# Kernel optimization log

Measured on AMD Instinct MI355X. Metric: run time of the kernel, lower is better.

Reference implementation:

```python
import math
import jax, jax.numpy as jnp
import numpy as np

B, T, D = 2, 2048, 1024
H, DH = 16, 64
DFF = int(4 * D * 2 / 3)  # 2730, as in the torch __init__
EPS = 1e-5


def _alibi_slopes(n_heads):
    def p2(n):
        start = 2 ** (-2 ** (-(math.log2(n) - 3)))
        return [start * start ** i for i in range(n)]
    if math.log2(n_heads).is_integer():
        s = p2(n_heads)
    else:
        closest = 2 ** math.floor(math.log2(n_heads))
        s = p2(closest) + p2(2 * closest)[0::2][: n_heads - closest]
    return jnp.asarray(s, dtype=jnp.float32)


def rmsnorm(x, g):
    var = jnp.mean(x * x, axis=-1, keepdims=True)
    return g * (x * jax.lax.rsqrt(var + EPS))


def setup_inputs() -> dict:
    key = jax.random.key(0)
    ks = jax.random.split(key, 9)
    sd = 0.02
    return {
        "x":  jax.random.normal(ks[0], (B, T, D), jnp.float32),
        "g1": jnp.ones((D,), jnp.float32),
        "Wq": jax.random.normal(ks[1], (D, H * DH), jnp.float32) * sd,
        "Wk": jax.random.normal(ks[2], (D, H * DH), jnp.float32) * sd,
        "Wv": jax.random.normal(ks[3], (D, H * DH), jnp.float32) * sd,
        "Wo": jax.random.normal(ks[4], (H * DH, D), jnp.float32) * sd,
        "g2": jnp.ones((D,), jnp.float32),
        "W1": jax.random.normal(ks[5], (D, DFF), jnp.float32) * sd,
        "W2": jax.random.normal(ks[6], (D, DFF), jnp.float32) * sd,
        "W3": jax.random.normal(ks[7], (DFF, D), jnp.float32) * sd,
    }


def reference(x, g1, Wq, Wk, Wv, Wo, g2, W1, W2, W3):
    scale = DH ** -0.5
    h = rmsnorm(x, g1)
    q = (h @ Wq).reshape(B, T, H, DH)
    k = (h @ Wk).reshape(B, T, H, DH)
    v = (h @ Wv).reshape(B, T, H, DH)
    # scores (B, H, T, T)
    att = jnp.einsum("bqhd,bkhd->bhqk", q, k) * scale
    # ALiBi bias as in source: dist = clamp(j - i, min=0) -> zero on causal region
    pos = jnp.arange(T)
    dist = jnp.clip(pos[None, :] - pos[:, None], 0, None).astype(jnp.float32)
    bias = -_alibi_slopes(H)[:, None, None] * dist[None, :, :]  # (H, T, T)
    causal = pos[None, :] <= pos[:, None]  # (T, T)
    neg_inf = jnp.asarray(-jnp.inf, att.dtype)
    att = jnp.where(causal[None, None], att + bias[None], neg_inf)
    p = jax.nn.softmax(att, axis=-1)
    ctx = jnp.einsum("bhqk,bkhd->bqhd", p, v).reshape(B, T, H * DH)
    x = x + ctx @ Wo
    h2 = rmsnorm(x, g2)
    x = x + (jax.nn.silu(h2 @ W1) * (h2 @ W2)) @ W3
    return x
```

## Files before the change

kernel.cpp:

```cpp
#include <hip/hip_runtime.h>
#include <hip/hip_bf16.h>
#include <cstdint>
#include <cstddef>

typedef __bf16 bf16;
typedef __attribute__((ext_vector_type(8))) __bf16 bf16x8;
typedef __attribute__((ext_vector_type(4))) float f32x4;

#define NB 2
#define NT 2048
#define ND 1024
#define NH 16
#define NDH 64
#define NBT 4096
#define NDFF 2730
#define NDFFP 2816
#define NQKV 3072
#define REPS 1e-5f
#define QK_SCALE_LOG2 0.1803368801111204f

#define AS1 __attribute__((address_space(1)))
#define AS3 __attribute__((address_space(3)))

#if __has_builtin(__builtin_amdgcn_exp2f)
#define EXP2F(x) __builtin_amdgcn_exp2f(x)
#else
#define EXP2F(x) exp2f(x)
#endif

__device__ __forceinline__ void g2l16(const bf16* g, bf16* l) {
    __builtin_amdgcn_global_load_lds((const AS1 uint32_t*)g, (AS3 uint32_t*)l, 16, 0, 0);
}

struct TPargs { const float* src[7]; bf16* dst[7]; };

__global__ void prep_weights_kernel(TPargs a) {
    __shared__ float tile[32][33];
    int bid = blockIdx.x;
    int idx, local, tilesX, K, N;
    if (bid < 4096) {
        idx = bid >> 10; local = bid & 1023; tilesX = 32; K = 1024; N = 1024;
    } else if (bid < 9728) {
        idx = 4 + (bid - 4096) / 2816; local = (bid - 4096) % 2816;
        tilesX = 32; K = 1024; N = 2730;
    } else {
        idx = 6; local = bid - 9728; tilesX = 88; K = 2730; N = 1024;
    }
    int Kp = tilesX * 32;
    int k0 = (local % tilesX) * 32;
    int n0 = (local / tilesX) * 32;
    const float* in = a.src[idx];
    bf16* out = a.dst[idx];
    int tx = threadIdx.x, ty = threadIdx.y;
#pragma unroll
    for (int j = 0; j < 4; ++j) {
        int k = k0 + ty + j * 8, n = n0 + tx;
        tile[ty + j * 8][tx] = (k < K && n < N) ? in[(size_t)k * N + n] : 0.0f;
    }
    __syncthreads();
#pragma unroll
    for (int j = 0; j < 4; ++j) {
        int n = n0 + ty + j * 8, k = k0 + tx;
        out[(size_t)n * Kp + k] = (bf16)tile[tx][ty + j * 8];
    }
}

__global__ void rmsnorm_kernel(const float* __restrict__ x, const float* __restrict__ g,
                               bf16* __restrict__ out) {
    int row = blockIdx.x;
    int t = threadIdx.x;
    const float4 v = reinterpret_cast<const float4*>(x + (size_t)row * ND)[t];
    float ss = v.x * v.x + v.y * v.y + v.z * v.z + v.w * v.w;
#pragma unroll
    for (int o = 32; o > 0; o >>= 1) ss += __shfl_down(ss, o, 64);
    __shared__ float red[4];
    if ((t & 63) == 0) red[t >> 6] = ss;
    __syncthreads();
    float scale = rsqrtf((red[0] + red[1] + red[2] + red[3]) * (1.0f / ND) + REPS);
    const float4 gv = reinterpret_cast<const float4*>(g)[t];
    union { bf16 b[4]; uint2 u; } pk;
    pk.b[0] = (bf16)(v.x * scale * gv.x);
    pk.b[1] = (bf16)(v.y * scale * gv.y);
    pk.b[2] = (bf16)(v.z * scale * gv.z);
    pk.b[3] = (bf16)(v.w * scale * gv.w);
    reinterpret_cast<uint2*>(out + (size_t)row * ND)[t] = pk.u;
}

__global__ __launch_bounds__(256)
void gemm_qkv_kernel(const bf16* __restrict__ A, const bf16* __restrict__ BT,
                     bf16* __restrict__ C, bf16* __restrict__ vt) {
    constexpr int K = ND, N = NQKV;
    __shared__ __align__(16) bf16 As[8192];
    __shared__ __align__(16) bf16 Bs[8192];
    int m0 = blockIdx.y * 128, n0 = blockIdx.x * 128;
    int t = threadIdx.x;
    int wave = t >> 6, lane = t & 63;
    int wr = (wave >> 1) * 64, wc = (wave & 1) * 64;
    int lm = lane & 15, quad = lane >> 4;

    f32x4 acc[4][4] = {};

    int r0 = t >> 2, c0 = (t & 3) * 8;
    const bf16* Ap = A + (size_t)(m0 + r0) * K + c0;
    const bf16* Bp = BT + (size_t)(n0 + r0) * K + c0;

    for (int k0 = 0; k0 < K; k0 += 64) {
        __syncthreads();
        g2l16(Ap + k0,                     As + t * 8);
        g2l16(Ap + (size_t)64 * K + k0,    As + 2048 + t * 8);
        g2l16(Ap + k0 + 32,                As + 4096 + t * 8);
        g2l16(Ap + (size_t)64 * K + k0 + 32, As + 6144 + t * 8);
        g2l16(Bp + k0,                     Bs + t * 8);
        g2l16(Bp + (size_t)64 * K + k0,    Bs + 2048 + t * 8);
        g2l16(Bp + k0 + 32,                Bs + 4096 + t * 8);
        g2l16(Bp + (size_t)64 * K + k0 + 32, Bs + 6144 + t * 8);
        __syncthreads();
#pragma unroll
        for (int ks = 0; ks < 2; ++ks) {
            bf16x8 af[4], bfr[4];
#pragma unroll
            for (int i = 0; i < 4; ++i)
                af[i] = *reinterpret_cast<const bf16x8*>(As + ks * 4096 + (wr + i * 16 + lm) * 32 + quad * 8);
#pragma unroll
            for (int j = 0; j < 4; ++j)
                bfr[j] = *reinterpret_cast<const bf16x8*>(Bs + ks * 4096 + (wc + j * 16 + lm) * 32 + quad * 8);
#pragma unroll
            for (int i = 0; i < 4; ++i)
#pragma unroll
                for (int j = 0; j < 4; ++j)
                    acc[i][j] = __builtin_amdgcn_mfma_f32_16x16x32_bf16(af[i], bfr[j], acc[i][j], 0, 0, 0);
        }
    }
    bool doVT = (n0 >= 2048);
#pragma unroll
    for (int i = 0; i < 4; ++i)
#pragma unroll
        for (int j = 0; j < 4; ++j) {
            int row0 = m0 + wr + i * 16 + quad * 4;
            int col = n0 + wc + j * 16 + lm;
            union { uint2 u2; bf16 e[4]; } pk;
#pragma unroll
            for (int r = 0; r < 4; ++r) {
                bf16 val = (bf16)acc[i][j][r];
                C[(size_t)(row0 + r) * N + col] = val;
                pk.e[r] = val;
            }
            if (doVT) {
                int cg = col - 2048;
                int h = cg >> 6, d = cg & 63;
                int b = row0 >> 11, t0 = row0 & 2047;
                *reinterpret_cast<uint2*>(vt + ((size_t)((b * 16 + h) * 64 + d)) * NT + t0) = pk.u2;
            }
        }
}

__global__ __launch_bounds__(256)
void gemm_ffn_kernel(const bf16* __restrict__ A, const bf16* __restrict__ BT,
                     bf16* __restrict__ Y) {
    constexpr int K = ND;
    __shared__ __align__(16) bf16 As[8192];
    __shared__ __align__(16) bf16 Bu[4096];
    __shared__ __align__(16) bf16 Bg[4096];
    int m0 = blockIdx.y * 128, n0 = blockIdx.x * 64;
    int t = threadIdx.x;
    int wave = t >> 6, lane = t & 63;
    int wr = (wave >> 1) * 64, wc = (wave & 1) * 32;
    int lm = lane & 15, quad = lane >> 4;

    f32x4 accU[4][2] = {};
    f32x4 accG[4][2] = {};

    int r0 = t >> 2, c0 = (t & 3) * 8;
    const bf16* Ap = A + (size_t)(m0 + r0) * K + c0;
    const bf16* Bup = BT + (size_t)(n0 + r0) * K + c0;
    const bf16* Bgp = BT + (size_t)(NDFFP + n0 + r0) * K + c0;

    for (int k0 = 0; k0 < K; k0 += 64) {
        __syncthreads();
        g2l16(Ap + k0,                       As + t * 8);
        g2l16(Ap + (size_t)64 * K + k0,      As + 2048 + t * 8);
        g2l16(Ap + k0 + 32,                  As + 4096 + t * 8);
        g2l16(Ap + (size_t)64 * K + k0 + 32, As + 6144 + t * 8);
        g2l16(Bup + k0,      Bu + t * 8);
        g2l16(Bup + k0 + 32, Bu + 2048 + t * 8);
        g2l16(Bgp + k0,      Bg + t * 8);
        g2l16(Bgp + k0 + 32, Bg + 2048 + t * 8);
        __syncthreads();
#pragma unroll
        for (int ks = 0; ks < 2; ++ks) {
            bf16x8 af[4], bu[2], bg[2];
#pragma unroll
            for (int i = 0; i < 4; ++i)
                af[i] = *reinterpret_cast<const bf16x8*>(As + ks * 4096 + (wr + i * 16 + lm) * 32 + quad * 8);
#pragma unroll
            for (int j = 0; j < 2; ++j) {
                bu[j] = *reinterpret_cast<const bf16x8*>(Bu + ks * 2048 + (wc + j * 16 + lm) * 32 + quad * 8);
                bg[j] = *reinterpret_cast<const bf16x8*>(Bg + ks * 2048 + (wc + j * 16 + lm) * 32 + quad * 8);
            }
#pragma unroll
            for (int i = 0; i < 4; ++i)
#pragma unroll
                for (int j = 0; j < 2; ++j) {
                    accU[i][j] = __builtin_amdgcn_mfma_f32_16x16x32_bf16(af[i], bu[j], accU[i][j], 0, 0, 0);
                    accG[i][j] = __builtin_amdgcn_mfma_f32_16x16x32_bf16(af[i], bg[j], accG[i][j], 0, 0, 0);
                }
        }
    }
#pragma unroll
    for (int i = 0; i < 4; ++i)
#pragma unroll
        for (int j = 0; j < 2; ++j)
#pragma unroll
            for (int r = 0; r < 4; ++r) {
                int row = m0 + wr + i * 16 + quad * 4 + r;
                int col = n0 + wc + j * 16 + lm;
                float u = accU[i][j][r], g = accG[i][j][r];
                float y = u / (1.0f + __expf(-u)) * g;
                Y[(size_t)row * NDFFP + col] = (bf16)y;
            }
}

__global__ __launch_bounds__(256)
void gemm_n64_kernel(const bf16* __restrict__ A, const bf16* __restrict__ BT,
                     float* __restrict__ C, const float* __restrict__ res,
                     int N, int K) {
    __shared__ __align__(16) bf16 As[8192];
    __shared__ __align__(16) bf16 Bs[4096];
    int m0 = blockIdx.y * 128, n0 = blockIdx.x * 64;
    int t = threadIdx.x;
    int wave = t >> 6, lane = t & 63;
    int wr = (wave >> 1) * 64, wc = (wave & 1) * 32;
    int lm = lane & 15, quad = lane >> 4;

    f32x4 acc[4][2] = {};

    int r0 = t >> 2, c0 = (t & 3) * 8;
    const bf16* Ap = A + (size_t)(m0 + r0) * K + c0;
    const bf16* Bp = BT + (size_t)(n0 + r0) * K + c0;

    for (int k0 = 0; k0 < K; k0 += 64) {
        __syncthreads();
        g2l16(Ap + k0,                       As + t * 8);
        g2l16(Ap + (size_t)64 * K + k0,      As + 2048 + t * 8);
        g2l16(Ap + k0 + 32,                  As + 4096 + t * 8);
        g2l16(Ap + (size_t)64 * K + k0 + 32, As + 6144 + t * 8);
        g2l16(Bp + k0,      Bs + t * 8);
        g2l16(Bp + k0 + 32, Bs + 2048 + t * 8);
        __syncthreads();
#pragma unroll
        for (int ks = 0; ks < 2; ++ks) {
            bf16x8 af[4], bfr[2];
#pragma unroll
            for (int i = 0; i < 4; ++i)
                af[i] = *reinterpret_cast<const bf16x8*>(As + ks * 4096 + (wr + i * 16 + lm) * 32 + quad * 8);
#pragma unroll
            for (int j = 0; j < 2; ++j)
                bfr[j] = *reinterpret_cast<const bf16x8*>(Bs + ks * 2048 + (wc + j * 16 + lm) * 32 + quad * 8);
#pragma unroll
            for (int i = 0; i < 4; ++i)
#pragma unroll
                for (int j = 0; j < 2; ++j)
                    acc[i][j] = __builtin_amdgcn_mfma_f32_16x16x32_bf16(af[i], bfr[j], acc[i][j], 0, 0, 0);
        }
    }
#pragma unroll
    for (int i = 0; i < 4; ++i)
#pragma unroll
        for (int j = 0; j < 2; ++j)
#pragma unroll
            for (int r = 0; r < 4; ++r) {
                int row = m0 + wr + i * 16 + quad * 4 + r;
                int col = n0 + wc + j * 16 + lm;
                C[(size_t)row * N + col] = res[(size_t)row * N + col] + acc[i][j][r];
            }
}

__global__ __launch_bounds__(256, 3)
void attn_kernel(const bf16* __restrict__ qkv, const bf16* __restrict__ vt,
                 bf16* __restrict__ ctx) {
    int bh = blockIdx.x;
    int qt = 31 - (int)blockIdx.y;
    int b = bh >> 4, h = bh & 15;
    int t = threadIdx.x, w = t >> 6, lane = t & 63;
    int lm = lane & 15, quad = lane >> 4;

    __shared__ __align__(16) bf16 Ks[2 * 4096];
    __shared__ __align__(16) bf16 VTs[4 * 2048];
    __shared__ __align__(16) bf16 Ps[4 * 16 * 136];

    const bf16* qbase = qkv + ((size_t)(b * NT + qt * 64)) * NQKV + h * 64;
    const bf16* kbase = qkv + ((size_t)b * NT) * NQKV + 1024 + h * 64;
    const bf16* vtb = vt + ((size_t)bh * 64) * NT;
    bf16* psw = Ps + w * 16 * 136;

    bf16x8 aq[2];
#pragma unroll
    for (int ks = 0; ks < 2; ++ks)
        aq[ks] = *reinterpret_cast<const bf16x8*>(
            qbase + (size_t)(w * 16 + lm) * NQKV + ks * 32 + quad * 8);

    f32x4 o[4] = {};
    float mrow[4] = {-1e30f, -1e30f, -1e30f, -1e30f};
    float lrow[4] = {0.f, 0.f, 0.f, 0.f};

    int nfull = qt >> 1;
    for (int kt = 0; kt <= nfull; ++kt) {
        int k0 = kt * 128;
        bool diag = (kt == nfull);
        __syncthreads();
#pragma unroll
        for (int rep = 0; rep < 4; ++rep) {
            int idx = (rep & 1) * 256 + t;
            int row = idx >> 2, ch = idx & 3;
            g2l16(kbase + (size_t)(k0 + row) * NQKV + (rep >> 1) * 32 + ch * 8,
                  Ks + (rep >> 1) * 4096 + idx * 8);
        }
#pragma unroll
        for (int rep = 0; rep < 4; ++rep) {
            int d = t >> 2, ch = t & 3;
            g2l16(vtb + (size_t)d * NT + k0 + rep * 32 + ch * 8,
                  VTs + rep * 2048 + t * 8);
        }
        __syncthreads();

        f32x4 s[8];
#pragma unroll
        for (int j = 0; j < 8; ++j) s[j] = f32x4{0.f, 0.f, 0.f, 0.f};
#pragma unroll
        for (int ks = 0; ks < 2; ++ks)
#pragma unroll
            for (int j = 0; j < 8; ++j) {
                bf16x8 bk = *reinterpret_cast<const bf16x8*>(
                    Ks + ks * 4096 + (j * 16 + lm) * 32 + quad * 8);
                s[j] = __builtin_amdgcn_mfma_f32_16x16x32_bf16(aq[ks], bk, s[j], 0, 0, 0);
            }
        if (diag) {
#pragma unroll
            for (int j = 0; j < 8; ++j) {
                int col = k0 + j * 16 + lm;
#pragma unroll
                for (int r = 0; r < 4; ++r) {
                    int row = qt * 64 + w * 16 + quad * 4 + r;
                    s[j][r] = (col > row) ? -1e30f : s[j][r] * QK_SCALE_LOG2;
                }
            }
        } else {
#pragma unroll
            for (int j = 0; j < 8; ++j)
#pragma unroll
                for (int r = 0; r < 4; ++r) s[j][r] *= QK_SCALE_LOG2;
        }
        float mx[4];
#pragma unroll
        for (int r = 0; r < 4; ++r) {
            float a = fmaxf(fmaxf(s[0][r], s[1][r]), fmaxf(s[2][r], s[3][r]));
            float c = fmaxf(fmaxf(s[4][r], s[5][r]), fmaxf(s[6][r], s[7][r]));
            mx[r] = fmaxf(a, c);
        }
#pragma unroll
        for (int d = 1; d < 16; d <<= 1)
#pragma unroll
            for (int r = 0; r < 4; ++r) mx[r] = fmaxf(mx[r], __shfl_xor(mx[r], d, 64));
        float al[4];
#pragma unroll
        for (int r = 0; r < 4; ++r) {
            float mn = fmaxf(mrow[r], mx[r]);
            al[r] = EXP2F(mrow[r] - mn);
            mrow[r] = mn;
        }
        float rsum[4] = {0.f, 0.f, 0.f, 0.f};
#pragma unroll
        for (int j = 0; j < 8; ++j)
#pragma unroll
            for (int r = 0; r < 4; ++r) {
                float pv = EXP2F(s[j][r] - mrow[r]);
                s[j][r] = pv;
                rsum[r] += pv;
            }
#pragma unroll
        for (int d = 1; d < 16; d <<= 1)
#pragma unroll
            for (int r = 0; r < 4; ++r) rsum[r] += __shfl_xor(rsum[r], d, 64);
#pragma unroll
        for (int r = 0; r < 4; ++r) lrow[r] = lrow[r] * al[r] + rsum[r];
#pragma unroll
        for (int n = 0; n < 4; ++n)
#pragma unroll
            for (int r = 0; r < 4; ++r) o[n][r] *= al[r];
#pragma unroll
        for (int j = 0; j < 8; ++j)
#pragma unroll
            for (int r = 0; r < 4; ++r)
                psw[(quad * 4 + r) * 136 + j * 16 + lm] = (bf16)s[j][r];
#pragma unroll
        for (int ks2 = 0; ks2 < 4; ++ks2) {
            bf16x8 ap = *reinterpret_cast<const bf16x8*>(psw + lm * 136 + ks2 * 32 + quad * 8);
#pragma unroll
            for (int n = 0; n < 4; ++n) {
                bf16x8 bv = *reinterpret_cast<const bf16x8*>(
                    VTs + ks2 * 2048 + (n * 16 + lm) * 32 + quad * 8);
                o[n] = __builtin_amdgcn_mfma_f32_16x16x32_bf16(ap, bv, o[n], 0, 0, 0);
            }
        }
    }
#pragma unroll
    for (int n = 0; n < 4; ++n)
#pragma unroll
        for (int r = 0; r < 4; ++r) {
            int row = qt * 64 + w * 16 + quad * 4 + r;
            ctx[((size_t)(b * NT + row)) * ND + h * 64 + n * 16 + lm] =
                (bf16)(o[n][r] / lrow[r]);
        }
}

extern "C" void kernel_launch(void* const* d_in, const int* in_sizes, int n_in,
                              void* d_out, int out_size, void* d_ws, size_t ws_size,
                              hipStream_t stream) {
    (void)in_sizes; (void)n_in; (void)out_size; (void)ws_size;
    const float* x  = (const float*)d_in[0];
    const float* g1 = (const float*)d_in[1];
    const float* g2 = (const float*)d_in[6];
    float* out = (float*)d_out;

    char* p = (char*)d_ws;
    auto take = [&](size_t n) { char* r = p; p += (n + 255) & ~(size_t)255; return r; };
    bf16* WqkvT = (bf16*)take((size_t)NQKV * ND * 2);
    bf16* WoT   = (bf16*)take((size_t)ND * ND * 2);
    bf16* W12T  = (bf16*)take((size_t)2 * NDFFP * ND * 2);
    bf16* W3T   = (bf16*)take((size_t)ND * NDFFP * 2);
    bf16* hb    = (bf16*)take((size_t)NBT * ND * 2);
    bf16* qkv   = (bf16*)take((size_t)NBT * NQKV * 2);
    bf16* vtb   = (bf16*)take((size_t)NB * NH * NDH * NT * 2);
    bf16* ctxb  = (bf16*)take((size_t)NBT * ND * 2);
    bf16* h2b   = (bf16*)take((size_t)NBT * ND * 2);
    bf16* ybuf  = qkv;

    TPargs tp;
    tp.src[0] = (const float*)d_in[2];  tp.dst[0] = WqkvT;
    tp.src[1] = (const float*)d_in[3];  tp.dst[1] = WqkvT + (size_t)ND * ND;
    tp.src[2] = (const float*)d_in[4];  tp.dst[2] = WqkvT + (size_t)2 * ND * ND;
    tp.src[3] = (const float*)d_in[5];  tp.dst[3] = WoT;
    tp.src[4] = (const float*)d_in[7];  tp.dst[4] = W12T;
    tp.src[5] = (const float*)d_in[8];  tp.dst[5] = W12T + (size_t)NDFFP * ND;
    tp.src[6] = (const float*)d_in[9];  tp.dst[6] = W3T;

    prep_weights_kernel<<<12544, dim3(32, 8), 0, stream>>>(tp);

    rmsnorm_kernel<<<NBT, 256, 0, stream>>>(x, g1, hb);

    gemm_qkv_kernel<<<dim3(24, 32), 256, 0, stream>>>(hb, WqkvT, qkv, vtb);

    attn_kernel<<<dim3(32, 32), 256, 0, stream>>>(qkv, vtb, ctxb);

    gemm_n64_kernel<<<dim3(16, 32), 256, 0, stream>>>(ctxb, WoT, out, x, ND, ND);

    rmsnorm_kernel<<<NBT, 256, 0, stream>>>(out, g2, h2b);

    gemm_ffn_kernel<<<dim3(44, 32), 256, 0, stream>>>(h2b, W12T, ybuf);

    gemm_n64_kernel<<<dim3(16, 32), 256, 0, stream>>>(ybuf, W3T, out, out, ND, NDFFP);
}
```

Measured before the change: 358.0 us.

## Fuse first RMSNorm into weight prep launch and halve FFN GEMM K-tile

Measured after the change: 355.4 us. About the same (-0.7%).

```diff
diff --git a/kernel.cpp b/kernel.cpp
--- a/kernel.cpp
+++ b/kernel.cpp
@@ -34,9 +34,31 @@
 
 struct TPargs { const float* src[7]; bf16* dst[7]; };
 
-__global__ void prep_weights_kernel(TPargs a) {
+__global__ __launch_bounds__(256)
+void prep_kernel(TPargs a, const float* __restrict__ x, const float* __restrict__ g1,
+                 bf16* __restrict__ hb) {
+    int bid = blockIdx.x;
+    int t = threadIdx.x;
+    if (bid >= 12544) {
+        int row = bid - 12544;
+        const float4 v = reinterpret_cast<const float4*>(x + (size_t)row * ND)[t];
+        float ss = v.x * v.x + v.y * v.y + v.z * v.z + v.w * v.w;
+#pragma unroll
+        for (int o = 32; o > 0; o >>= 1) ss += __shfl_down(ss, o, 64);
+        __shared__ float red[4];
+        if ((t & 63) == 0) red[t >> 6] = ss;
+        __syncthreads();
+        float scale = rsqrtf((red[0] + red[1] + red[2] + red[3]) * (1.0f / ND) + REPS);
+        const float4 gv = reinterpret_cast<const float4*>(g1)[t];
+        union { bf16 b[4]; uint2 u; } pk;
+        pk.b[0] = (bf16)(v.x * scale * gv.x);
+        pk.b[1] = (bf16)(v.y * scale * gv.y);
+        pk.b[2] = (bf16)(v.z * scale * gv.z);
+        pk.b[3] = (bf16)(v.w * scale * gv.w);
+        reinterpret_cast<uint2*>(hb + (size_t)row * ND)[t] = pk.u;
+        return;
+    }
     __shared__ float tile[32][33];
-    int bid = blockIdx.x;
     int idx, local, tilesX, K, N;
     if (bid < 4096) {
         idx = bid >> 10; local = bid & 1023; tilesX = 32; K = 1024; N = 1024;
@@ -51,7 +73,7 @@
     int n0 = (local / tilesX) * 32;
     const float* in = a.src[idx];
     bf16* out = a.dst[idx];
-    int tx = threadIdx.x, ty = threadIdx.y;
+    int tx = t & 31, ty = t >> 5;
 #pragma unroll
     for (int j = 0; j < 4; ++j) {
         int k = k0 + ty + j * 8, n = n0 + tx;
@@ -158,9 +180,9 @@
 void gemm_ffn_kernel(const bf16* __restrict__ A, const bf16* __restrict__ BT,
                      bf16* __restrict__ Y) {
     constexpr int K = ND;
-    __shared__ __align__(16) bf16 As[8192];
-    __shared__ __align__(16) bf16 Bu[4096];
-    __shared__ __align__(16) bf16 Bg[4096];
+    __shared__ __align__(16) bf16 As[4096];
+    __shared__ __align__(16) bf16 Bu[2048];
+    __shared__ __align__(16) bf16 Bg[2048];
     int m0 = blockIdx.y * 128, n0 = blockIdx.x * 64;
     int t = threadIdx.x;
     int wave = t >> 6, lane = t & 63;
@@ -175,36 +197,29 @@
     const bf16* Bup = BT + (size_t)(n0 + r0) * K + c0;
     const bf16* Bgp = BT + (size_t)(NDFFP + n0 + r0) * K + c0;
 
-    for (int k0 = 0; k0 < K; k0 += 64) {
-        __syncthreads();
-        g2l16(Ap + k0,                       As + t * 8);
-        g2l16(Ap + (size_t)64 * K + k0,      As + 2048 + t * 8);
-        g2l16(Ap + k0 + 32,                  As + 4096 + t * 8);
-        g2l16(Ap + (size_t)64 * K + k0 + 32, As + 6144 + t * 8);
-        g2l16(Bup + k0,      Bu + t * 8);
-        g2l16(Bup + k0 + 32, Bu + 2048 + t * 8);
-        g2l16(Bgp + k0,      Bg + t * 8);
-        g2l16(Bgp + k0 + 32, Bg + 2048 + t * 8);
-        __syncthreads();
-#pragma unroll
-        for (int ks = 0; ks < 2; ++ks) {
-            bf16x8 af[4], bu[2], bg[2];
-#pragma unroll
-            for (int i = 0; i < 4; ++i)
-                af[i] = *reinterpret_cast<const bf16x8*>(As + ks * 4096 + (wr + i * 16 + lm) * 32 + quad * 8);
+    for (int k0 = 0; k0 < K; k0 += 32) {
+        __syncthreads();
+        g2l16(Ap + k0, As + t * 8);
+        g2l16(Ap + (size_t)64 * K + k0, As + 2048 + t * 8);
+        g2l16(Bup + k0, Bu + t * 8);
+        g2l16(Bgp + k0, Bg + t * 8);
+        __syncthreads();
+        bf16x8 af[4], bu[2], bg[2];
+#pragma unroll
+        for (int i = 0; i < 4; ++i)
+            af[i] = *reinterpret_cast<const bf16x8*>(As + (wr + i * 16 + lm) * 32 + quad * 8);
+#pragma unroll
+        for (int j = 0; j < 2; ++j) {
+            bu[j] = *reinterpret_cast<const bf16x8*>(Bu + (wc + j * 16 + lm) * 32 + quad * 8);
+            bg[j] = *reinterpret_cast<const bf16x8*>(Bg + (wc + j * 16 + lm) * 32 + quad * 8);
+        }
+#pragma unroll
+        for (int i = 0; i < 4; ++i)
 #pragma unroll
             for (int j = 0; j < 2; ++j) {
-                bu[j] = *reinterpret_cast<const bf16x8*>(Bu + ks * 2048 + (wc + j * 16 + lm) * 32 + quad * 8);
-                bg[j] = *reinterpret_cast<const bf16x8*>(Bg + ks * 2048 + (wc + j * 16 + lm) * 32 + quad * 8);
-            }
-#pragma unroll
-            for (int i = 0; i < 4; ++i)
-#pragma unroll
-                for (int j = 0; j < 2; ++j) {
-                    accU[i][j] = __builtin_amdgcn_mfma_f32_16x16x32_bf16(af[i], bu[j], accU[i][j], 0, 0, 0);
-                    accG[i][j] = __builtin_amdgcn_mfma_f32_16x16x32_bf16(af[i], bg[j], accG[i][j], 0, 0, 0);
-                }
-        }
+                accU[i][j] = __builtin_amdgcn_mfma_f32_16x16x32_bf16(af[i], bu[j], accU[i][j], 0, 0, 0);
+                accG[i][j] = __builtin_amdgcn_mfma_f32_16x16x32_bf16(af[i], bg[j], accG[i][j], 0, 0, 0);
+            }
     }
 #pragma unroll
     for (int i = 0; i < 4; ++i)
@@ -444,9 +459,7 @@
     tp.src[5] = (const float*)d_in[8];  tp.dst[5] = W12T + (size_t)NDFFP * ND;
     tp.src[6] = (const float*)d_in[9];  tp.dst[6] = W3T;
 
-    prep_weights_kernel<<<12544, dim3(32, 8), 0, stream>>>(tp);
-
-    rmsnorm_kernel<<<NBT, 256, 0, stream>>>(x, g1, hb);
+    prep_kernel<<<12544 + NBT, 256, 0, stream>>>(tp, x, g1, hb);
 
     gemm_qkv_kernel<<<dim3(24, 32), 256, 0, stream>>>(hb, WqkvT, qkv, vtb);
 
```
